# Kernel optimization log

Measured on AMD Instinct MI355X. Metric: run time of the kernel, lower is better.

## Reference

```python
import jax, jax.numpy as jnp
import numpy as np

B, LS, LL, D, H, T = 32, 256, 256, 2048, 16, 1000
TAU = 0.07


def setup_inputs():
    key = jax.random.key(0)
    k = jax.random.split(key, 9)
    embed_seq = jax.random.normal(k[0], (B, LS, D), jnp.float32)
    embed_label = jax.random.normal(k[1], (B, LL, D), jnp.float32)
    noise = jax.random.normal(k[2], (B, LS + LL, D), jnp.float32)
    timestep = jax.random.randint(k[3], (B,), 0, T)
    # DDPM linear schedule buffers (betas init arg = [1e-4, 0.02] endpoints)
    betas = jnp.linspace(1e-4, 0.02, T, dtype=jnp.float32)
    ac = jnp.cumprod(1.0 - betas)
    sqrt_alphas_cumprod = jnp.sqrt(ac)
    sqrt_one_minus_alphas_cumprod = jnp.sqrt(1.0 - ac)
    s = 1.0 / np.sqrt(D).astype(np.float32)
    Wq = jax.random.normal(k[4], (D, D), jnp.float32) * s
    Wk = jax.random.normal(k[5], (D, D), jnp.float32) * s
    Wv = jax.random.normal(k[6], (D, D), jnp.float32) * s
    Wo = jax.random.normal(k[7], (D, D), jnp.float32) * s
    return {
        "embed_seq": embed_seq,
        "embed_label": embed_label,
        "noise": noise,
        "sqrt_alphas_cumprod": sqrt_alphas_cumprod,
        "sqrt_one_minus_alphas_cumprod": sqrt_one_minus_alphas_cumprod,
        "Wq": Wq,
        "Wk": Wk,
        "Wv": Wv,
        "Wo": Wo,
        "timestep": timestep,
    }


def _mha(x, Wq, Wk, Wv, Wo):
    # ProteinFuncAttention denoiser: standard MHSA with d_model=D, n_header=H
    b, s, _ = x.shape
    dh = D // H
    q = (x @ Wq).reshape(b, s, H, dh)
    kk = (x @ Wk).reshape(b, s, H, dh)
    v = (x @ Wv).reshape(b, s, H, dh)
    scores = jnp.einsum("bqhd,bkhd->bhqk", q, kk) / np.sqrt(dh).astype(np.float32)
    attn = jax.nn.softmax(scores, axis=-1)
    out = jnp.einsum("bhqk,bkhd->bqhd", attn, v).reshape(b, s, D)
    return out @ Wo


def _contrast_all_channels(f1, f2):
    # f1: [D,B,L], f2: [D,B,L] -> vectorized per-channel cosine-sim + CE(diag)
    sim = jnp.einsum("dik,djk->dij", f1, f2)  # [D,B,B]
    n1 = jnp.linalg.norm(f1, axis=-1)  # [D,B]
    n2 = jnp.linalg.norm(f2, axis=-1)  # [D,B]
    logits = sim / (n1[:, :, None] * n2[:, None, :]) / TAU
    lse = jax.scipy.special.logsumexp(logits, axis=-1)  # [D,B]
    diag = jnp.diagonal(logits, axis1=1, axis2=2)  # [D,B]
    # sum_d( mean_b(ce_d) ) / D  ==  mean over (d,b)
    return jnp.mean(lse - diag)


def reference(embed_seq, embed_label, noise, sqrt_alphas_cumprod,
              sqrt_one_minus_alphas_cumprod, Wq, Wk, Wv, Wo, timestep):
    x_start = jnp.concatenate([embed_seq, embed_label], axis=1)  # [B,LS+LL,D]
    # q_sample
    sa = sqrt_alphas_cumprod[timestep][:, None, None]
    s1m = sqrt_one_minus_alphas_cumprod[timestep][:, None, None]
    x_t = sa * x_start + s1m * noise
    model_output = _mha(x_t, Wq, Wk, Wv, Wo)
    # mean_flat(...).mean() over equal-sized batch == global mean
    mse_loss = jnp.mean((x_start - model_output) ** 2)
    out_mean = sqrt_alphas_cumprod[T - 1] * x_start
    tT_loss = jnp.mean(out_mean ** 2)
    # per-channel contrastive losses, vectorized with D as batch dim
    f_seq = jnp.transpose(x_start[:, :LS, :], (2, 0, 1))  # [D,B,LS]
    f_lab = jnp.transpose(x_start[:, LS:, :], (2, 0, 1))  # [D,B,LL]
    match_loss = _contrast_all_channels(f_seq, f_lab)
    ctr_loss = _contrast_all_channels(f_lab, f_lab)
    return mse_loss + tT_loss + match_loss + ctr_loss
```

## Files before the change

### kernel.cpp

```cpp
#include <hip/hip_runtime.h>
#include <stdint.h>

#define B_    32
#define L_    512
#define D_    2048
#define H_    16
#define M_    16384
#define NQKV_ 6144
#define TAU_INV 14.285714285714286f
#define LOG2E   1.4426950408889634f
#define SCALE_Q 0.08838834764831845f

using f32x4 = __attribute__((ext_vector_type(4))) float;
using s16x8 = __attribute__((ext_vector_type(8))) short;

__device__ __forceinline__ uint16_t f2bf(float f){
  uint32_t u = __float_as_uint(f);
  uint32_t r = (u + 0x7fffu + ((u >> 16) & 1u)) >> 16;
  return (uint16_t)r;
}

__device__ __forceinline__ void async16(const void* g, void* s){
  __builtin_amdgcn_global_load_lds((const __attribute__((address_space(1))) void*)g,
                                   (__attribute__((address_space(3))) void*)s, 16, 0, 0);
}

__global__ void k_prep(const float* __restrict__ sac, const float* __restrict__ s1m,
                       const int* __restrict__ ts, float* __restrict__ scal,
                       double* __restrict__ accs){
  int t = threadIdx.x;
  if (t < 32){ int tt = ts[t]; scal[t] = sac[tt]; scal[32 + t] = s1m[tt]; }
  if (t == 64){ float v = sac[999]; scal[64] = v * v; }
  if (t >= 96 && t < 104) accs[t - 96] = 0.0;
}

__launch_bounds__(256)
__global__ void k_convw(const float* __restrict__ wq, const float* __restrict__ wk,
                        const float* __restrict__ wv, const float* __restrict__ wo,
                        uint16_t* __restrict__ wqkv_t, uint16_t* __restrict__ wo_t){
  int w = blockIdx.z;
  const float* src = (w == 0) ? wq : (w == 1) ? wk : (w == 2) ? wv : wo;
  uint16_t* dst = (w < 3) ? (wqkv_t + (size_t)w * D_ * D_) : wo_t;
  float scale = (w == 0) ? SCALE_Q : 1.0f;
  __shared__ float tile[64][65];
  int n0 = blockIdx.x * 64, k0 = blockIdx.y * 64;
  int tx = threadIdx.x & 15, ty = threadIdx.x >> 4;
  #pragma unroll
  for (int r = 0; r < 4; r++){
    int kk = ty + r * 16;
    float4 v = *(const float4*)&src[(size_t)(k0 + kk) * D_ + n0 + tx * 4];
    tile[kk][tx*4+0] = v.x; tile[kk][tx*4+1] = v.y;
    tile[kk][tx*4+2] = v.z; tile[kk][tx*4+3] = v.w;
  }
  __syncthreads();
  #pragma unroll
  for (int r = 0; r < 4; r++){
    int nn = ty + r * 16;
    ushort4 o;
    o.x = f2bf(tile[tx*4+0][nn] * scale);
    o.y = f2bf(tile[tx*4+1][nn] * scale);
    o.z = f2bf(tile[tx*4+2][nn] * scale);
    o.w = f2bf(tile[tx*4+3][nn] * scale);
    *(ushort4*)&dst[(size_t)(n0 + nn) * D_ + k0 + tx * 4] = o;
  }
}

__launch_bounds__(256)
__global__ void k_xt(const float* __restrict__ seq, const float* __restrict__ lab,
                     const float* __restrict__ noise, const float* __restrict__ scal,
                     double* __restrict__ accs, uint16_t* __restrict__ xt){
  __shared__ float red[4];
  int tid = threadIdx.x;
  size_t base = ((size_t)blockIdx.x * 256 + tid) * 8;
  int b = (int)(base >> 20);
  int rem = (int)(base & 1048575u);
  int l = rem >> 11, d0 = rem & 2047;
  const float* xsp = (l < 256) ? seq + ((size_t)(b * 256 + l) << 11) + d0
                               : lab + ((size_t)(b * 256 + l - 256) << 11) + d0;
  float4 x0 = *(const float4*)xsp;
  float4 x1 = *(const float4*)(xsp + 4);
  float4 n0 = *(const float4*)(noise + base);
  float4 n1 = *(const float4*)(noise + base + 4);
  float sa = scal[b], sm = scal[32 + b];
  ushort4 o0, o1;
  o0.x = f2bf(sa*x0.x + sm*n0.x); o0.y = f2bf(sa*x0.y + sm*n0.y);
  o0.z = f2bf(sa*x0.z + sm*n0.z); o0.w = f2bf(sa*x0.w + sm*n0.w);
  o1.x = f2bf(sa*x1.x + sm*n1.x); o1.y = f2bf(sa*x1.y + sm*n1.y);
  o1.z = f2bf(sa*x1.z + sm*n1.z); o1.w = f2bf(sa*x1.w + sm*n1.w);
  *(ushort4*)(xt + base) = o0;
  *(ushort4*)(xt + base + 4) = o1;
  float s2 = x0.x*x0.x + x0.y*x0.y + x0.z*x0.z + x0.w*x0.w
           + x1.x*x1.x + x1.y*x1.y + x1.z*x1.z + x1.w*x1.w;
  #pragma unroll
  for (int m = 32; m >= 1; m >>= 1){ s2 += __shfl_xor(s2, m); }
  if ((tid & 63) == 0) red[tid >> 6] = s2;
  __syncthreads();
  if (tid == 0) atomicAdd(&accs[0], (double)(red[0] + red[1] + red[2] + red[3]));
}

template<int MODE>
__launch_bounds__(256)
__global__ void k_gemm(const uint16_t* __restrict__ A, const uint16_t* __restrict__ Bt,
                       uint16_t* __restrict__ oq, uint16_t* __restrict__ ok,
                       uint16_t* __restrict__ ovt,
                       const float* __restrict__ seq, const float* __restrict__ lab,
                       double* __restrict__ accs){
  __shared__ __align__(16) uint16_t As[128 * 32];
  __shared__ __align__(16) uint16_t Bs[128 * 32];
  __shared__ float red[4];
  const int tid = threadIdx.x;
  const int lane = tid & 63;
  const int wv = tid >> 6, wr = wv >> 1, wc = wv & 1;
  const int r16 = lane & 15, g4 = lane >> 4;
  const int brow = blockIdx.y * 128;
  const int bcol = blockIdx.x * 128;
  const int rowA0 = tid >> 2, p0 = tid & 3;
  const int rowA1 = rowA0 + 64;
  const int sw0 = (p0 ^ (rowA0 & 3)) * 8;
  const int sw1 = (p0 ^ (rowA1 & 3)) * 8;
  const int swr = (g4 ^ (r16 & 3)) * 8;

  const f32x4 z4 = {0.f, 0.f, 0.f, 0.f};
  f32x4 acc[4][4];
  #pragma unroll
  for (int i = 0; i < 4; i++){
    #pragma unroll
    for (int j = 0; j < 4; j++){ acc[i][j] = z4; }
  }

  for (int k0 = 0; k0 < 2048; k0 += 32){
    if (MODE == 0){
      async16(A + (size_t)(brow + rowA0) * 2048 + k0 + sw0, &As[rowA0 * 32 + p0 * 8]);
      async16(A + (size_t)(brow + rowA1) * 2048 + k0 + sw1, &As[rowA1 * 32 + p0 * 8]);
    } else {
      const int hh = k0 >> 7, dhb = k0 & 127;
      const int m0 = brow + rowA0, m1 = brow + rowA1;
      async16(A + (size_t)(((m0 >> 9) * 16 + hh) * 512 + (m0 & 511)) * 128 + dhb + sw0,
              &As[rowA0 * 32 + p0 * 8]);
      async16(A + (size_t)(((m1 >> 9) * 16 + hh) * 512 + (m1 & 511)) * 128 + dhb + sw1,
              &As[rowA1 * 32 + p0 * 8]);
    }
    async16(Bt + (size_t)(bcol + rowA0) * 2048 + k0 + sw0, &Bs[rowA0 * 32 + p0 * 8]);
    async16(Bt + (size_t)(bcol + rowA1) * 2048 + k0 + sw1, &Bs[rowA1 * 32 + p0 * 8]);
    __syncthreads();
    s16x8 af[4], bfr[4];
    #pragma unroll
    for (int i = 0; i < 4; i++){
      af[i] = *(const s16x8*)&As[(wr * 64 + i * 16 + r16) * 32 + swr];
    }
    #pragma unroll
    for (int j = 0; j < 4; j++){
      bfr[j] = *(const s16x8*)&Bs[(wc * 64 + j * 16 + r16) * 32 + swr];
    }
    #pragma unroll
    for (int i = 0; i < 4; i++){
      #pragma unroll
      for (int j = 0; j < 4; j++){
        acc[i][j] = __builtin_amdgcn_mfma_f32_16x16x32_bf16(af[i], bfr[j], acc[i][j], 0, 0, 0);
      }
    }
    __syncthreads();
  }

  if (MODE == 0){
    #pragma unroll
    for (int i = 0; i < 4; i++){
      const int m = brow + wr * 64 + i * 16 + g4 * 4;
      const int bb = m >> 9, lbase = m & 511;
      #pragma unroll
      for (int j = 0; j < 4; j++){
        const int n = bcol + wc * 64 + j * 16 + r16;
        const int which = n >> 11, nn = n & 2047;
        const int hh = nn >> 7, dh = nn & 127;
        if (which == 2){
          ushort4 ov;
          ov.x = f2bf(acc[i][j][0]); ov.y = f2bf(acc[i][j][1]);
          ov.z = f2bf(acc[i][j][2]); ov.w = f2bf(acc[i][j][3]);
          *(ushort4*)&ovt[((size_t)((bb * 16 + hh) * 128 + dh)) * 512 + lbase] = ov;
        } else {
          uint16_t* dst = (which == 0) ? oq : ok;
          #pragma unroll
          for (int r = 0; r < 4; r++){
            dst[((size_t)((bb * 16 + hh) * 512 + lbase + r)) * 128 + dh] = f2bf(acc[i][j][r]);
          }
        }
      }
    }
  } else {
    float msum = 0.f;
    #pragma unroll
    for (int i = 0; i < 4; i++){
      const int m = brow + wr * 64 + i * 16 + g4 * 4;
      const int bb = m >> 9;
      #pragma unroll
      for (int j = 0; j < 4; j++){
        const int n = bcol + wc * 64 + j * 16 + r16;
        #pragma unroll
        for (int r = 0; r < 4; r++){
          const int l = (m + r) & 511;
          const float xs = (l < 256)
              ? seq[((size_t)(bb * 256 + l)) * 2048 + n]
              : lab[((size_t)(bb * 256 + l - 256)) * 2048 + n];
          const float d = xs - acc[i][j][r];
          msum += d * d;
        }
      }
    }
    #pragma unroll
    for (int s = 32; s >= 1; s >>= 1){ msum += __shfl_xor(msum, s); }
    if (lane == 0) red[wv] = msum;
    __syncthreads();
    if (tid == 0) atomicAdd(&accs[1], (double)(red[0] + red[1] + red[2] + red[3]));
  }
}

__launch_bounds__(256)
__global__ void k_attn(const uint16_t* __restrict__ q, const uint16_t* __restrict__ kk,
                       const uint16_t* __restrict__ vt, uint16_t* __restrict__ o){
  __shared__ __align__(16) uint16_t Ks[64 * 128];
  __shared__ __align__(16) uint16_t Vs[128 * 64];
  __shared__ __align__(16) uint16_t Ps[4][32][72];
  const int tid = threadIdx.x, lane = tid & 63, wv = tid >> 6;
  const int r16 = lane & 15, g4 = lane >> 4;
  const int bid = blockIdx.x;
  const int qb = bid & 3, hh = (bid >> 2) & 15, bb = bid >> 6;
  const size_t head = (size_t)(bb * 16 + hh) * 512 * 128;
  const int q0 = qb * 128 + wv * 32;

  const f32x4 z4 = {0.f, 0.f, 0.f, 0.f};
  s16x8 aq[2][4];
  #pragma unroll
  for (int mi = 0; mi < 2; mi++){
    #pragma unroll
    for (int kb = 0; kb < 4; kb++){
      aq[mi][kb] = *(const s16x8*)&q[head + (size_t)(q0 + mi * 16 + r16) * 128 + kb * 32 + g4 * 8];
    }
  }
  f32x4 oacc[2][8];
  #pragma unroll
  for (int mi = 0; mi < 2; mi++){
    #pragma unroll
    for (int nf = 0; nf < 8; nf++){ oacc[mi][nf] = z4; }
  }
  f32x4 mrun[2], lrun[2];
  const f32x4 minit = {-1e30f, -1e30f, -1e30f, -1e30f};
  mrun[0] = minit; mrun[1] = minit; lrun[0] = z4; lrun[1] = z4;

  for (int t = 0; t < 8; t++){
    const int kv0 = t * 64;
    #pragma unroll
    for (int it = 0; it < 4; it++){
      const int s = it * 256 + tid;
      const int row = s >> 4, p = s & 15;
      const int pg = p ^ (row & 7);
      async16(kk + head + (size_t)(kv0 + row) * 128 + pg * 8, &Ks[s * 8]);
    }
    #pragma unroll
    for (int it = 0; it < 4; it++){
      const int s = it * 256 + tid;
      const int row = s >> 3, p = s & 7;
      const int pg = p ^ (row & 7);
      async16(vt + head + (size_t)row * 512 + kv0 + pg * 8, &Vs[s * 8]);
    }
    __syncthreads();

    f32x4 sf[2][4];
    #pragma unroll
    for (int mi = 0; mi < 2; mi++){
      #pragma unroll
      for (int nj = 0; nj < 4; nj++){ sf[mi][nj] = z4; }
    }
    #pragma unroll
    for (int kb = 0; kb < 4; kb++){
      #pragma unroll
      for (int nj = 0; nj < 4; nj++){
        const int krow = nj * 16 + r16;
        const s16x8 bk = *(const s16x8*)&Ks[krow * 128 + (((kb * 4 + g4) ^ (krow & 7)) * 8)];
        sf[0][nj] = __builtin_amdgcn_mfma_f32_16x16x32_bf16(aq[0][kb], bk, sf[0][nj], 0, 0, 0);
        sf[1][nj] = __builtin_amdgcn_mfma_f32_16x16x32_bf16(aq[1][kb], bk, sf[1][nj], 0, 0, 0);
      }
    }
    #pragma unroll
    for (int mi = 0; mi < 2; mi++){
      float sc[4];
      #pragma unroll
      for (int r = 0; r < 4; r++){
        float v = fmaxf(fmaxf(sf[mi][0][r], sf[mi][1][r]), fmaxf(sf[mi][2][r], sf[mi][3][r]));
        v = fmaxf(v, __shfl_xor(v, 1));
        v = fmaxf(v, __shfl_xor(v, 2));
        v = fmaxf(v, __shfl_xor(v, 4));
        v = fmaxf(v, __shfl_xor(v, 8));
        const float mold = mrun[mi][r];
        const float mnew = fmaxf(mold, v);
        sc[r] = exp2f((mold - mnew) * LOG2E);
        mrun[mi][r] = mnew;
      }
      float ps[4] = {0.f, 0.f, 0.f, 0.f};
      #pragma unroll
      for (int nj = 0; nj < 4; nj++){
        #pragma unroll
        for (int r = 0; r < 4; r++){
          const float p = exp2f((sf[mi][nj][r] - mrun[mi][r]) * LOG2E);
          ps[r] += p;
          Ps[wv][mi * 16 + g4 * 4 + r][nj * 16 + r16] = f2bf(p);
        }
      }
      #pragma unroll
      for (int r = 0; r < 4; r++){
        float v = ps[r];
        v += __shfl_xor(v, 1); v += __shfl_xor(v, 2);
        v += __shfl_xor(v, 4); v += __shfl_xor(v, 8);
        lrun[mi][r] = lrun[mi][r] * sc[r] + v;
      }
      #pragma unroll
      for (int nf = 0; nf < 8; nf++){
        #pragma unroll
        for (int r = 0; r < 4; r++){ oacc[mi][nf][r] *= sc[r]; }
      }
    }
    #pragma unroll
    for (int kc = 0; kc < 2; kc++){
      const s16x8 ap0 = *(const s16x8*)&Ps[wv][r16][kc * 32 + g4 * 8];
      const s16x8 ap1 = *(const s16x8*)&Ps[wv][16 + r16][kc * 32 + g4 * 8];
      #pragma unroll
      for (int nf = 0; nf < 8; nf++){
        const int dh = nf * 16 + r16;
        const s16x8 bv = *(const s16x8*)&Vs[dh * 64 + (((kc * 4 + g4) ^ (dh & 7)) * 8)];
        oacc[0][nf] = __builtin_amdgcn_mfma_f32_16x16x32_bf16(ap0, bv, oacc[0][nf], 0, 0, 0);
        oacc[1][nf] = __builtin_amdgcn_mfma_f32_16x16x32_bf16(ap1, bv, oacc[1][nf], 0, 0, 0);
      }
    }
    __syncthreads();
  }
  #pragma unroll
  for (int mi = 0; mi < 2; mi++){
    #pragma unroll
    for (int r = 0; r < 4; r++){
      const float inv = 1.0f / lrun[mi][r];
      const size_t rowbase = head + (size_t)(q0 + mi * 16 + g4 * 4 + r) * 128;
      #pragma unroll
      for (int nf = 0; nf < 8; nf++){
        o[rowbase + nf * 16 + r16] = f2bf(oacc[mi][nf][r] * inv);
      }
    }
  }
}

__launch_bounds__(256)
__global__ void k_contrast(const float* __restrict__ seq, const float* __restrict__ lab,
                           double* __restrict__ accs){
  __shared__ float ss[8][32][8];
  __shared__ float ls[8][32][8];
  __shared__ float rsl[32][8];
  __shared__ float redM[4], redC[4];
  const int tid = threadIdx.x, lane = tid & 63, wv = tid >> 6;
  const int i = tid >> 3, dd = tid & 7;
  const int d = blockIdx.x * 8 + dd;
  float accM[32], accC[32];
  #pragma unroll
  for (int j = 0; j < 32; j++){ accM[j] = 0.f; accC[j] = 0.f; }
  float accS = 0.f, accL = 0.f;
  for (int l0 = 0; l0 < 256; l0 += 8){
    #pragma unroll
    for (int li = 0; li < 8; li++){
      ss[li][i][dd] = seq[((size_t)(i * 256 + l0 + li)) * 2048 + d];
      ls[li][i][dd] = lab[((size_t)(i * 256 + l0 + li)) * 2048 + d];
    }
    __syncthreads();
    #pragma unroll
    for (int li = 0; li < 8; li++){
      const float sv = ss[li][i][dd];
      const float lv = ls[li][i][dd];
      accS += sv * sv; accL += lv * lv;
      #pragma unroll
      for (int j = 0; j < 32; j++){
        const float lj = ls[li][j][dd];
        accM[j] += sv * lj;
        accC[j] += lv * lj;
      }
    }
    __syncthreads();
  }
  rsl[i][dd] = rsqrtf(accL);
  __syncthreads();
  const float rs1 = rsqrtf(accS);
  const float rso = rsl[i][dd];
  float mx = -1e30f, diag = 0.f;
  #pragma unroll
  for (int j = 0; j < 32; j++){
    const float lg = accM[j] * rs1 * rsl[j][dd] * TAU_INV;
    mx = fmaxf(mx, lg);
    if (j == i) diag = lg;
  }
  float sum = 0.f;
  #pragma unroll
  for (int j = 0; j < 32; j++){
    const float lg = accM[j] * rs1 * rsl[j][dd] * TAU_INV;
    sum += exp2f((lg - mx) * LOG2E);
  }
  const float lossM = mx + logf(sum) - diag;
  mx = -1e30f; diag = 0.f;
  #pragma unroll
  for (int j = 0; j < 32; j++){
    const float lg = accC[j] * rso * rsl[j][dd] * TAU_INV;
    mx = fmaxf(mx, lg);
    if (j == i) diag = lg;
  }
  sum = 0.f;
  #pragma unroll
  for (int j = 0; j < 32; j++){
    const float lg = accC[j] * rso * rsl[j][dd] * TAU_INV;
    sum += exp2f((lg - mx) * LOG2E);
  }
  const float lossC = mx + logf(sum) - diag;

  float vM = lossM, vC = lossC;
  #pragma unroll
  for (int s = 32; s >= 1; s >>= 1){ vM += __shfl_xor(vM, s); vC += __shfl_xor(vC, s); }
  if (lane == 0){ redM[wv] = vM; redC[wv] = vC; }
  __syncthreads();
  if (tid == 0){
    atomicAdd(&accs[2], (double)(redM[0] + redM[1] + redM[2] + redM[3]));
    atomicAdd(&accs[3], (double)(redC[0] + redC[1] + redC[2] + redC[3]));
  }
}

__global__ void k_final(const float* __restrict__ scal, const double* __restrict__ accs,
                        float* __restrict__ out){
  if (threadIdx.x == 0){
    const double inv = 1.0 / ((double)M_ * (double)D_);
    double v = accs[1] * inv
             + (double)scal[64] * accs[0] * inv
             + accs[2] / 65536.0
             + accs[3] / 65536.0;
    out[0] = (float)v;
  }
}

extern "C" void kernel_launch(void* const* d_in, const int* in_sizes, int n_in,
                              void* d_out, int out_size, void* d_ws, size_t ws_size,
                              hipStream_t stream){
  const float* seq   = (const float*)d_in[0];
  const float* lab   = (const float*)d_in[1];
  const float* noise = (const float*)d_in[2];
  const float* sac   = (const float*)d_in[3];
  const float* s1m   = (const float*)d_in[4];
  const float* wq    = (const float*)d_in[5];
  const float* wk    = (const float*)d_in[6];
  const float* wvp   = (const float*)d_in[7];
  const float* wo    = (const float*)d_in[8];
  const int*   ts    = (const int*)d_in[9];

  char* ws = (char*)d_ws;
  float*    scal = (float*)ws;
  double*   accs = (double*)(ws + 512);
  uint16_t* wqkv = (uint16_t*)(ws + 1024);
  uint16_t* wo_t = wqkv + (size_t)NQKV_ * D_;
  uint16_t* xt   = wo_t + (size_t)D_ * D_;
  uint16_t* qb   = xt + (size_t)M_ * D_;
  uint16_t* kb   = qb + (size_t)M_ * D_;
  uint16_t* vtb  = kb + (size_t)M_ * D_;
  float* out = (float*)d_out;

  k_prep<<<1, 128, 0, stream>>>(sac, s1m, ts, scal, accs);
  k_convw<<<dim3(32, 32, 4), 256, 0, stream>>>(wq, wk, wvp, wo, wqkv, wo_t);
  k_xt<<<16384, 256, 0, stream>>>(seq, lab, noise, scal, accs, xt);
  k_gemm<0><<<dim3(48, 128), 256, 0, stream>>>(xt, wqkv, qb, kb, vtb, nullptr, nullptr, nullptr);
  k_attn<<<2048, 256, 0, stream>>>(qb, kb, vtb, xt);
  k_gemm<1><<<dim3(16, 128), 256, 0, stream>>>(xt, wo_t, nullptr, nullptr, nullptr, seq, lab, accs);
  k_contrast<<<256, 256, 0, stream>>>(seq, lab, accs);
  k_final<<<1, 64, 0, stream>>>(scal, accs, out);
}
```

Before: 1.437 ms.

## Use 256x256 double-buffered GEMM tiles and pipeline attention KV loads

Replaces the 128x128 single-buffered GEMM with a 256x256-tile, 512-thread kernel. It double-buffers LDS with K-steps of 64, interleaves async global->LDS loads with MFMA, uses s_setprio, and remaps workgroups into XCD-aware order. The attention kernel now double-buffers K/V in 32-row chunks, prefetching the next chunk while computing on the current one. The aim is to hide memory latency, raise arithmetic intensity per tile and improve L2 locality, at the cost of more registers and LDS per block and lower occupancy.

```diff
diff --git a/kernel.cpp b/kernel.cpp
--- a/kernel.cpp
+++ b/kernel.cpp
@@ -99,89 +99,135 @@
 }
 
 template<int MODE>
-__launch_bounds__(256)
-__global__ void k_gemm(const uint16_t* __restrict__ A, const uint16_t* __restrict__ Bt,
-                       uint16_t* __restrict__ oq, uint16_t* __restrict__ ok,
-                       uint16_t* __restrict__ ovt,
-                       const float* __restrict__ seq, const float* __restrict__ lab,
-                       double* __restrict__ accs){
-  __shared__ __align__(16) uint16_t As[128 * 32];
-  __shared__ __align__(16) uint16_t Bs[128 * 32];
-  __shared__ float red[4];
-  const int tid = threadIdx.x;
-  const int lane = tid & 63;
-  const int wv = tid >> 6, wr = wv >> 1, wc = wv & 1;
+__launch_bounds__(512, 2)
+__global__ void k_gemm256(const uint16_t* __restrict__ A, const uint16_t* __restrict__ Bt,
+                          uint16_t* __restrict__ oq, uint16_t* __restrict__ ok,
+                          uint16_t* __restrict__ ovt,
+                          const float* __restrict__ seq, const float* __restrict__ lab,
+                          double* __restrict__ accs){
+  __shared__ __align__(16) uint16_t lds[2][4][256 * 32];
+  __shared__ float red[8];
+  const int tid = threadIdx.x, lane = tid & 63, wid = tid >> 6;
+  const int wr = wid >> 2, wc = wid & 3;
   const int r16 = lane & 15, g4 = lane >> 4;
-  const int brow = blockIdx.y * 128;
-  const int bcol = blockIdx.x * 128;
-  const int rowA0 = tid >> 2, p0 = tid & 3;
-  const int rowA1 = rowA0 + 64;
-  const int sw0 = (p0 ^ (rowA0 & 3)) * 8;
-  const int sw1 = (p0 ^ (rowA1 & 3)) * 8;
-  const int swr = (g4 ^ (r16 & 3)) * 8;
+  const int NX = (MODE == 0) ? 24 : 8;
+  const int nwg = (MODE == 0) ? 1536 : 512;
+  const int id = blockIdx.x;
+  const int wgs = (id & 7) * (nwg >> 3) + (id >> 3);
+  const int by = wgs / NX, bx = wgs % NX;
+  const int brow = by * 256, bcol = bx * 256;
+
+  int srow[2], gp8[2], dstoff[2];
+  #pragma unroll
+  for (int i = 0; i < 2; i++){
+    int s = i * 512 + tid;
+    srow[i] = s >> 2;
+    gp8[i] = (((s & 3) ^ ((srow[i] >> 1) & 3)) << 3);
+    dstoff[i] = s * 8;
+  }
+
+  auto stageA = [&](int t, int s, int b){
+    #pragma unroll
+    for (int i = 0; i < 2; i++){
+      const uint16_t* src;
+      if (MODE == 0){
+        src = A + (size_t)(brow + srow[i]) * 2048 + t * 64 + s * 32 + gp8[i];
+      } else {
+        int m = brow + srow[i];
+        src = A + (size_t)(((m >> 9) * 16 + (t >> 1)) * 512 + (m & 511)) * 128
+                + (t & 1) * 64 + s * 32 + gp8[i];
+      }
+      async16(src, &lds[b][2 * s][dstoff[i]]);
+    }
+  };
+  auto stageB = [&](int t, int s, int b){
+    #pragma unroll
+    for (int i = 0; i < 2; i++){
+      async16(Bt + (size_t)(bcol + srow[i]) * 2048 + t * 64 + s * 32 + gp8[i],
+              &lds[b][2 * s + 1][dstoff[i]]);
+    }
+  };
+
+  const int rsw = (r16 >> 1) & 3;
+  int aoff[8], boff[4];
+  #pragma unroll
+  for (int mf = 0; mf < 8; mf++){
+    aoff[mf] = (wr * 128 + mf * 16 + r16) * 32 + ((g4 ^ rsw) << 3);
+  }
+  #pragma unroll
+  for (int nf = 0; nf < 4; nf++){
+    boff[nf] = (wc * 64 + nf * 16 + r16) * 32 + ((g4 ^ rsw) << 3);
+  }
 
   const f32x4 z4 = {0.f, 0.f, 0.f, 0.f};
-  f32x4 acc[4][4];
-  #pragma unroll
-  for (int i = 0; i < 4; i++){
+  f32x4 acc[8][4];
+  #pragma unroll
+  for (int i = 0; i < 8; i++){
     #pragma unroll
     for (int j = 0; j < 4; j++){ acc[i][j] = z4; }
   }
 
-  for (int k0 = 0; k0 < 2048; k0 += 32){
-    if (MODE == 0){
-      async16(A + (size_t)(brow + rowA0) * 2048 + k0 + sw0, &As[rowA0 * 32 + p0 * 8]);
-      async16(A + (size_t)(brow + rowA1) * 2048 + k0 + sw1, &As[rowA1 * 32 + p0 * 8]);
-    } else {
-      const int hh = k0 >> 7, dhb = k0 & 127;
-      const int m0 = brow + rowA0, m1 = brow + rowA1;
-      async16(A + (size_t)(((m0 >> 9) * 16 + hh) * 512 + (m0 & 511)) * 128 + dhb + sw0,
-              &As[rowA0 * 32 + p0 * 8]);
-      async16(A + (size_t)(((m1 >> 9) * 16 + hh) * 512 + (m1 & 511)) * 128 + dhb + sw1,
-              &As[rowA1 * 32 + p0 * 8]);
-    }
-    async16(Bt + (size_t)(bcol + rowA0) * 2048 + k0 + sw0, &Bs[rowA0 * 32 + p0 * 8]);
-    async16(Bt + (size_t)(bcol + rowA1) * 2048 + k0 + sw1, &Bs[rowA1 * 32 + p0 * 8]);
-    __syncthreads();
-    s16x8 af[4], bfr[4];
-    #pragma unroll
-    for (int i = 0; i < 4; i++){
-      af[i] = *(const s16x8*)&As[(wr * 64 + i * 16 + r16) * 32 + swr];
-    }
-    #pragma unroll
-    for (int j = 0; j < 4; j++){
-      bfr[j] = *(const s16x8*)&Bs[(wc * 64 + j * 16 + r16) * 32 + swr];
-    }
-    #pragma unroll
-    for (int i = 0; i < 4; i++){
-      #pragma unroll
-      for (int j = 0; j < 4; j++){
-        acc[i][j] = __builtin_amdgcn_mfma_f32_16x16x32_bf16(af[i], bfr[j], acc[i][j], 0, 0, 0);
-      }
-    }
-    __syncthreads();
+  stageA(0, 0, 0); stageB(0, 0, 0); stageA(0, 1, 0); stageB(0, 1, 0);
+  asm volatile("s_waitcnt vmcnt(4)" ::: "memory");
+  __builtin_amdgcn_s_barrier();
+
+  for (int t = 0; t < 32; t++){
+    const int c = t & 1, nb = c ^ 1, tn = (t + 1) & 31;
+    #pragma unroll
+    for (int s = 0; s < 2; s++){
+      s16x8 bfrag[4], afrag[4];
+      #pragma unroll
+      for (int nf = 0; nf < 4; nf++) bfrag[nf] = *(const s16x8*)&lds[c][2*s+1][boff[nf]];
+      #pragma unroll
+      for (int mf = 0; mf < 4; mf++) afrag[mf] = *(const s16x8*)&lds[c][2*s][aoff[mf]];
+      stageA(tn, s, nb);
+      __builtin_amdgcn_s_setprio(1);
+      #pragma unroll
+      for (int mf = 0; mf < 4; mf++){
+        #pragma unroll
+        for (int nf = 0; nf < 4; nf++){
+          acc[mf][nf] = __builtin_amdgcn_mfma_f32_16x16x32_bf16(afrag[mf], bfrag[nf], acc[mf][nf], 0, 0, 0);
+        }
+      }
+      __builtin_amdgcn_s_setprio(0);
+      __builtin_amdgcn_s_barrier();
+      #pragma unroll
+      for (int mf = 0; mf < 4; mf++) afrag[mf] = *(const s16x8*)&lds[c][2*s][aoff[4+mf]];
+      stageB(tn, s, nb);
+      asm volatile("s_waitcnt vmcnt(4)" ::: "memory");
+      __builtin_amdgcn_s_setprio(1);
+      #pragma unroll
+      for (int mf = 0; mf < 4; mf++){
+        #pragma unroll
+        for (int nf = 0; nf < 4; nf++){
+          acc[4+mf][nf] = __builtin_amdgcn_mfma_f32_16x16x32_bf16(afrag[mf], bfrag[nf], acc[4+mf][nf], 0, 0, 0);
+        }
+      }
+      __builtin_amdgcn_s_setprio(0);
+      __builtin_amdgcn_s_barrier();
+    }
   }
 
   if (MODE == 0){
     #pragma unroll
-    for (int i = 0; i < 4; i++){
-      const int m = brow + wr * 64 + i * 16 + g4 * 4;
+    for (int mf = 0; mf < 8; mf++){
+      const int m = brow + wr * 128 + mf * 16 + g4 * 4;
       const int bb = m >> 9, lbase = m & 511;
       #pragma unroll
-      for (int j = 0; j < 4; j++){
-        const int n = bcol + wc * 64 + j * 16 + r16;
+      for (int nf = 0; nf < 4; nf++){
+        const int n = bcol + wc * 64 + nf * 16 + r16;
         const int which = n >> 11, nn = n & 2047;
         const int hh = nn >> 7, dh = nn & 127;
         if (which == 2){
           ushort4 ov;
-          ov.x = f2bf(acc[i][j][0]); ov.y = f2bf(acc[i][j][1]);
-          ov.z = f2bf(acc[i][j][2]); ov.w = f2bf(acc[i][j][3]);
+          ov.x = f2bf(acc[mf][nf][0]); ov.y = f2bf(acc[mf][nf][1]);
+          ov.z = f2bf(acc[mf][nf][2]); ov.w = f2bf(acc[mf][nf][3]);
           *(ushort4*)&ovt[((size_t)((bb * 16 + hh) * 128 + dh)) * 512 + lbase] = ov;
         } else {
           uint16_t* dst = (which == 0) ? oq : ok;
           #pragma unroll
           for (int r = 0; r < 4; r++){
-            dst[((size_t)((bb * 16 + hh) * 512 + lbase + r)) * 128 + dh] = f2bf(acc[i][j][r]);
+            dst[((size_t)((bb * 16 + hh) * 512 + lbase + r)) * 128 + dh] = f2bf(acc[mf][nf][r]);
           }
         }
       }
@@ -189,36 +235,41 @@
   } else {
     float msum = 0.f;
     #pragma unroll
-    for (int i = 0; i < 4; i++){
-      const int m = brow + wr * 64 + i * 16 + g4 * 4;
+    for (int mf = 0; mf < 8; mf++){
+      const int m = brow + wr * 128 + mf * 16 + g4 * 4;
       const int bb = m >> 9;
       #pragma unroll
-      for (int j = 0; j < 4; j++){
-        const int n = bcol + wc * 64 + j * 16 + r16;
+      for (int nf = 0; nf < 4; nf++){
+        const int n = bcol + wc * 64 + nf * 16 + r16;
         #pragma unroll
         for (int r = 0; r < 4; r++){
           const int l = (m + r) & 511;
           const float xs = (l < 256)
               ? seq[((size_t)(bb * 256 + l)) * 2048 + n]
               : lab[((size_t)(bb * 256 + l - 256)) * 2048 + n];
-          const float d = xs - acc[i][j][r];
+          const float d = xs - acc[mf][nf][r];
           msum += d * d;
         }
       }
     }
     #pragma unroll
-    for (int s = 32; s >= 1; s >>= 1){ msum += __shfl_xor(msum, s); }
-    if (lane == 0) red[wv] = msum;
+    for (int sh = 32; sh >= 1; sh >>= 1){ msum += __shfl_xor(msum, sh); }
+    if (lane == 0) red[wid] = msum;
     __syncthreads();
-    if (tid == 0) atomicAdd(&accs[1], (double)(red[0] + red[1] + red[2] + red[3]));
+    if (tid == 0){
+      float tot = 0.f;
+      #pragma unroll
+      for (int i = 0; i < 8; i++) tot += red[i];
+      atomicAdd(&accs[1], (double)tot);
+    }
   }
 }
 
 __launch_bounds__(256)
 __global__ void k_attn(const uint16_t* __restrict__ q, const uint16_t* __restrict__ kk,
                        const uint16_t* __restrict__ vt, uint16_t* __restrict__ o){
-  __shared__ __align__(16) uint16_t Ks[64 * 128];
-  __shared__ __align__(16) uint16_t Vs[128 * 64];
+  __shared__ __align__(16) uint16_t Ks[2][32 * 128];
+  __shared__ __align__(16) uint16_t Vs[2][128 * 32];
   __shared__ __align__(16) uint16_t Ps[4][32][72];
   const int tid = threadIdx.x, lane = tid & 63, wv = tid >> 6;
   const int r16 = lane & 15, g4 = lane >> 4;
@@ -246,36 +297,41 @@
   const f32x4 minit = {-1e30f, -1e30f, -1e30f, -1e30f};
   mrun[0] = minit; mrun[1] = minit; lrun[0] = z4; lrun[1] = z4;
 
-  for (int t = 0; t < 8; t++){
-    const int kv0 = t * 64;
-    #pragma unroll
-    for (int it = 0; it < 4; it++){
-      const int s = it * 256 + tid;
-      const int row = s >> 4, p = s & 15;
-      const int pg = p ^ (row & 7);
-      async16(kk + head + (size_t)(kv0 + row) * 128 + pg * 8, &Ks[s * 8]);
-    }
-    #pragma unroll
-    for (int it = 0; it < 4; it++){
-      const int s = it * 256 + tid;
-      const int row = s >> 3, p = s & 7;
-      const int pg = p ^ (row & 7);
-      async16(vt + head + (size_t)row * 512 + kv0 + pg * 8, &Vs[s * 8]);
-    }
-    __syncthreads();
-
-    f32x4 sf[2][4];
-    #pragma unroll
-    for (int mi = 0; mi < 2; mi++){
-      #pragma unroll
-      for (int nj = 0; nj < 4; nj++){ sf[mi][nj] = z4; }
-    }
+  auto stageKV = [&](int t, int b){
+    const int kv0 = t * 32;
+    #pragma unroll
+    for (int it = 0; it < 2; it++){
+      int s = it * 256 + tid;
+      int row = s >> 4, p = s & 15;
+      async16(kk + head + (size_t)(kv0 + row) * 128 + ((p ^ (row & 7)) << 3), &Ks[b][s * 8]);
+    }
+    #pragma unroll
+    for (int it = 0; it < 2; it++){
+      int s = it * 256 + tid;
+      int row = s >> 2, p = s & 3;
+      async16(vt + head + (size_t)row * 512 + kv0 + ((p ^ ((row >> 1) & 3)) << 3), &Vs[b][s * 8]);
+    }
+  };
+
+  stageKV(0, 0);
+  for (int t = 0; t < 16; t++){
+    const int c = t & 1;
+    if (t < 15){
+      stageKV(t + 1, c ^ 1);
+      asm volatile("s_waitcnt vmcnt(4)" ::: "memory");
+    } else {
+      asm volatile("s_waitcnt vmcnt(0)" ::: "memory");
+    }
+    __builtin_amdgcn_s_barrier();
+
+    f32x4 sf[2][2];
+    sf[0][0] = z4; sf[0][1] = z4; sf[1][0] = z4; sf[1][1] = z4;
     #pragma unroll
     for (int kb = 0; kb < 4; kb++){
       #pragma unroll
-      for (int nj = 0; nj < 4; nj++){
+      for (int nj = 0; nj < 2; nj++){
         const int krow = nj * 16 + r16;
-        const s16x8 bk = *(const s16x8*)&Ks[krow * 128 + (((kb * 4 + g4) ^ (krow & 7)) * 8)];
+        const s16x8 bk = *(const s16x8*)&Ks[c][krow * 128 + ((((kb * 4 + g4) ^ (krow & 7))) << 3)];
         sf[0][nj] = __builtin_amdgcn_mfma_f32_16x16x32_bf16(aq[0][kb], bk, sf[0][nj], 0, 0, 0);
         sf[1][nj] = __builtin_amdgcn_mfma_f32_16x16x32_bf16(aq[1][kb], bk, sf[1][nj], 0, 0, 0);
       }
@@ -285,7 +341,7 @@
       float sc[4];
       #pragma unroll
       for (int r = 0; r < 4; r++){
-        float v = fmaxf(fmaxf(sf[mi][0][r], sf[mi][1][r]), fmaxf(sf[mi][2][r], sf[mi][3][r]));
+        float v = fmaxf(sf[mi][0][r], sf[mi][1][r]);
         v = fmaxf(v, __shfl_xor(v, 1));
         v = fmaxf(v, __shfl_xor(v, 2));
         v = fmaxf(v, __shfl_xor(v, 4));
@@ -297,7 +353,7 @@
       }
       float ps[4] = {0.f, 0.f, 0.f, 0.f};
       #pragma unroll
-      for (int nj = 0; nj < 4; nj++){
+      for (int nj = 0; nj < 2; nj++){
         #pragma unroll
         for (int r = 0; r < 4; r++){
           const float p = exp2f((sf[mi][nj][r] - mrun[mi][r]) * LOG2E);
@@ -318,19 +374,16 @@
         for (int r = 0; r < 4; r++){ oacc[mi][nf][r] *= sc[r]; }
       }
     }
-    #pragma unroll
-    for (int kc = 0; kc < 2; kc++){
-      const s16x8 ap0 = *(const s16x8*)&Ps[wv][r16][kc * 32 + g4 * 8];
-      const s16x8 ap1 = *(const s16x8*)&Ps[wv][16 + r16][kc * 32 + g4 * 8];
-      #pragma unroll
-      for (int nf = 0; nf < 8; nf++){
-        const int dh = nf * 16 + r16;
-        const s16x8 bv = *(const s16x8*)&Vs[dh * 64 + (((kc * 4 + g4) ^ (dh & 7)) * 8)];
-        oacc[0][nf] = __builtin_amdgcn_mfma_f32_16x16x32_bf16(ap0, bv, oacc[0][nf], 0, 0, 0);
-        oacc[1][nf] = __builtin_amdgcn_mfma_f32_16x16x32_bf16(ap1, bv, oacc[1][nf], 0, 0, 0);
-      }
-    }
-    __syncthreads();
+    const s16x8 ap0 = *(const s16x8*)&Ps[wv][r16][g4 * 8];
+    const s16x8 ap1 = *(const s16x8*)&Ps[wv][16 + r16][g4 * 8];
+    #pragma unroll
+    for (int nf = 0; nf < 8; nf++){
+      const int dh = nf * 16 + r16;
+      const s16x8 bv = *(const s16x8*)&Vs[c][dh * 32 + ((g4 ^ ((dh >> 1) & 3)) << 3)];
+      oacc[0][nf] = __builtin_amdgcn_mfma_f32_16x16x32_bf16(ap0, bv, oacc[0][nf], 0, 0, 0);
+      oacc[1][nf] = __builtin_amdgcn_mfma_f32_16x16x32_bf16(ap1, bv, oacc[1][nf], 0, 0, 0);
+    }
+    __builtin_amdgcn_s_barrier();
   }
   #pragma unroll
   for (int mi = 0; mi < 2; mi++){
@@ -465,9 +518,9 @@
   k_prep<<<1, 128, 0, stream>>>(sac, s1m, ts, scal, accs);
   k_convw<<<dim3(32, 32, 4), 256, 0, stream>>>(wq, wk, wvp, wo, wqkv, wo_t);
   k_xt<<<16384, 256, 0, stream>>>(seq, lab, noise, scal, accs, xt);
-  k_gemm<0><<<dim3(48, 128), 256, 0, stream>>>(xt, wqkv, qb, kb, vtb, nullptr, nullptr, nullptr);
+  k_gemm256<0><<<1536, 512, 0, stream>>>(xt, wqkv, qb, kb, vtb, nullptr, nullptr, nullptr);
   k_attn<<<2048, 256, 0, stream>>>(qb, kb, vtb, xt);
-  k_gemm<1><<<dim3(16, 128), 256, 0, stream>>>(xt, wo_t, nullptr, nullptr, nullptr, seq, lab, accs);
+  k_gemm256<1><<<512, 512, 0, stream>>>(xt, wo_t, nullptr, nullptr, nullptr, seq, lab, accs);
   k_contrast<<<256, 256, 0, stream>>>(seq, lab, accs);
   k_final<<<1, 64, 0, stream>>>(scal, accs, out);
 }
```

After: 1.353 ms. 5.8% less time.
